# Kernel tuning notes

Measured on AMD Instinct MI355X. Metric: run time of the kernel, lower is better.

## Reference

```python
import jax, jax.numpy as jnp
import numpy as np

N = 100000      # nodes
E = 1600000     # edges (avg degree 16)
IN_DIM = 128
HID = 128
OUT = 10
EPS = 1e-5      # BatchNorm eps


def _lin(key, fan_in, fan_out):
    return jax.random.normal(key, (fan_in, fan_out), jnp.float32) * (1.0 / np.sqrt(fan_in))


def setup_inputs() -> dict:
    key = jax.random.key(0)
    ks = jax.random.split(key, 8)
    x = jax.random.normal(ks[0], (N, IN_DIM), jnp.float32)
    edge_index = jax.random.randint(ks[1], (2, E), 0, N, dtype=jnp.int64)
    return {
        "x": x,
        "edge_index": edge_index,
        "W0": _lin(ks[2], IN_DIM, HID), "b0": jnp.zeros((HID,), jnp.float32),
        "g0": jnp.ones((HID,), jnp.float32), "be0": jnp.zeros((HID,), jnp.float32),
        "W1": _lin(ks[3], HID, HID), "b1": jnp.zeros((HID,), jnp.float32),
        "g1": jnp.ones((HID,), jnp.float32), "be1": jnp.zeros((HID,), jnp.float32),
        "W2": _lin(ks[4], HID, OUT), "b2": jnp.zeros((OUT,), jnp.float32),
    }


def gcn_conv(x, W, b, src, dst, n):
    # PyG GCNConv: add self-loops, symmetric normalization D^-1/2 A D^-1/2.
    # deg includes the self-loop (+1).
    e = src.shape[0]
    deg = jax.ops.segment_sum(jnp.ones((e,), x.dtype), dst, num_segments=n) + 1.0
    dinv = jax.lax.rsqrt(deg)                     # deg >= 1 always
    norm = dinv[src] * dinv[dst]                  # [E]
    h = x @ W                                     # [N, out]
    msgs = h[src] * norm[:, None]                 # gather + scale, [E, out]
    agg = jax.ops.segment_sum(msgs, dst, num_segments=n)
    agg = agg + h * (dinv * dinv)[:, None]        # self-loop contribution
    return agg + b


def batch_norm(x, gamma, beta):
    mu = jnp.mean(x, axis=0)
    var = jnp.mean(jnp.square(x - mu), axis=0)    # biased var, as torch BN training
    return gamma * (x - mu) * jax.lax.rsqrt(var + EPS) + beta


def reference(x, edge_index, W0, b0, g0, be0, W1, b1, g1, be1, W2, b2):
    src, dst = edge_index[0], edge_index[1]
    h = jax.nn.relu(batch_norm(gcn_conv(x, W0, b0, src, dst, N), g0, be0))
    h = jax.nn.relu(batch_norm(gcn_conv(h, W1, b1, src, dst, N), g1, be1))
    return gcn_conv(h, W2, b2, src, dst, N)
```

## Files before the change

kernel.cpp:

```cpp
#include <hip/hip_runtime.h>
#include <hip/hip_bf16.h>

static constexpr int NN  = 100000;
static constexpr int NE  = 1600000;
static constexpr int DIM = 128;
static constexpr int OC  = 10;
static constexpr int BK  = 64;
static constexpr float BN_EPS = 1e-5f;
static constexpr float INVN   = 1.0f / (float)NN;

typedef unsigned short ushortT;
typedef unsigned int uintT;
typedef __attribute__((ext_vector_type(8))) short short8;
typedef __attribute__((ext_vector_type(4))) float floatx4;

__device__ __forceinline__ ushortT f2bf(float f) {
    union { float f; unsigned int i; } c;
    c.f = f;
    unsigned int r = c.i + 0x7FFFu + ((c.i >> 16) & 1u);
    return (ushortT)(r >> 16);
}

__device__ __forceinline__ uintT pack2(float lo, float hi) {
    return (uintT)f2bf(lo) | ((uintT)f2bf(hi) << 16);
}

__device__ __forceinline__ float4 f4fma(const float4 w, const float s, const float4 acc) {
    float4 r;
    r.x = fmaf(w.x, s, acc.x);
    r.y = fmaf(w.y, s, acc.y);
    r.z = fmaf(w.z, s, acc.z);
    r.w = fmaf(w.w, s, acc.w);
    return r;
}

__device__ __forceinline__ void acc8(const uint4 u, float* a) {
    a[0] += __uint_as_float(u.x << 16);
    a[1] += __uint_as_float(u.x & 0xFFFF0000u);
    a[2] += __uint_as_float(u.y << 16);
    a[3] += __uint_as_float(u.y & 0xFFFF0000u);
    a[4] += __uint_as_float(u.z << 16);
    a[5] += __uint_as_float(u.z & 0xFFFF0000u);
    a[6] += __uint_as_float(u.w << 16);
    a[7] += __uint_as_float(u.w & 0xFFFF0000u);
}

__device__ __forceinline__ void fma8(const uint4 u, float s, float* a) {
    a[0] = fmaf(__uint_as_float(u.x << 16),          s, a[0]);
    a[1] = fmaf(__uint_as_float(u.x & 0xFFFF0000u),  s, a[1]);
    a[2] = fmaf(__uint_as_float(u.y << 16),          s, a[2]);
    a[3] = fmaf(__uint_as_float(u.y & 0xFFFF0000u),  s, a[3]);
    a[4] = fmaf(__uint_as_float(u.z << 16),          s, a[4]);
    a[5] = fmaf(__uint_as_float(u.z & 0xFFFF0000u),  s, a[5]);
    a[6] = fmaf(__uint_as_float(u.w << 16),          s, a[6]);
    a[7] = fmaf(__uint_as_float(u.w & 0xFFFF0000u),  s, a[7]);
}

__device__ __forceinline__ void unp8(const uint4 u, float* a) {
    a[0] = __uint_as_float(u.x << 16);
    a[1] = __uint_as_float(u.x & 0xFFFF0000u);
    a[2] = __uint_as_float(u.y << 16);
    a[3] = __uint_as_float(u.y & 0xFFFF0000u);
    a[4] = __uint_as_float(u.z << 16);
    a[5] = __uint_as_float(u.z & 0xFFFF0000u);
    a[6] = __uint_as_float(u.w << 16);
    a[7] = __uint_as_float(u.w & 0xFFFF0000u);
}

__global__ void k_wt(const float* __restrict__ W0, const float* __restrict__ W1,
                     ushortT* __restrict__ WT0, ushortT* __restrict__ WT1,
                     float* __restrict__ stats) {
    int i = blockIdx.x * 256 + threadIdx.x;
    if (i < 512) stats[i] = 0.f;
    int half = i >> 14, r = i & 16383;
    int n = r >> 7, k = r & 127;
    if (half == 0) WT0[r] = f2bf(W0[k * 128 + n]);
    else           WT1[r] = f2bf(W1[k * 128 + n]);
}

__global__ __launch_bounds__(256, 8)
void k_fused(const int* __restrict__ src, const int* __restrict__ dst,
             int* __restrict__ cnt, int* __restrict__ bucket,
             const float* __restrict__ x, const ushortT* __restrict__ WT,
             ushortT* __restrict__ outb)
{
    const int idx = blockIdx.x;
    const int m = idx / 3, r3 = idx - 3 * m;
    if (r3 < 2) {
        int e = (2 * m + r3) * 256 + threadIdx.x;
        if (e < NE) {
            int t = dst[e];
            int slot = atomicAdd(&cnt[t], 1);
            if (slot < BK)
                __hip_atomic_store(&bucket[(size_t)t * BK + slot], src[e],
                                   __ATOMIC_RELAXED, __HIP_MEMORY_SCOPE_AGENT);
        }
        return;
    }
    __shared__ ushortT XS[32 * 136];
    const int tid  = threadIdx.x;
    const int row0 = m * 32;

    #pragma unroll
    for (int i = 0; i < 4; ++i) {
        int id2 = tid + 256 * i;
        int rr = id2 >> 5, c4 = id2 & 31;
        int grow = row0 + rr;
        float4 v = {0.f, 0.f, 0.f, 0.f};
        if (grow < NN) v = ((const float4*)(x + (size_t)grow * DIM))[c4];
        ushort4 o;
        o.x = f2bf(v.x); o.y = f2bf(v.y); o.z = f2bf(v.z); o.w = f2bf(v.w);
        *(ushort4*)(XS + rr * 136 + c4 * 4) = o;
    }
    __syncthreads();

    const int w    = tid >> 6;
    const int lane = tid & 63;
    const int q    = lane >> 4;
    const int mr   = lane & 15;
    const int rw   = (w >> 1) * 16;
    const int ch   = (w & 1) * 64;

    floatx4 acc[4];
    #pragma unroll
    for (int t = 0; t < 4; ++t) { acc[t][0] = 0.f; acc[t][1] = 0.f; acc[t][2] = 0.f; acc[t][3] = 0.f; }

    #pragma unroll
    for (int c = 0; c < 4; ++c) {
        short8 a = *(const short8*)(XS + (rw + mr) * 136 + c * 32 + q * 8);
        #pragma unroll
        for (int t = 0; t < 4; ++t) {
            short8 b = *(const short8*)(WT + (size_t)(ch + t * 16 + mr) * 128 + c * 32 + q * 8);
            acc[t] = __builtin_amdgcn_mfma_f32_16x16x32_bf16(a, b, acc[t], 0, 0, 0);
        }
    }

    #pragma unroll
    for (int rr = 0; rr < 4; ++rr) {
        int grow = row0 + rw + q * 4 + rr;
        if (grow < NN) {
            #pragma unroll
            for (int t = 0; t < 4; ++t)
                outb[(size_t)grow * DIM + ch + t * 16 + mr] = f2bf(acc[t][rr]);
        }
    }
}

__global__ void k_dinv(const int* __restrict__ cnt, float* __restrict__ dinv, int n) {
    int i = blockIdx.x * 256 + threadIdx.x;
    if (i < n) dinv[i] = rsqrtf((float)cnt[i] + 1.0f);
}

template <bool EDGE_SCALE>
__global__ __launch_bounds__(256)
void k_agg_wide(const ushortT* __restrict__ hb, const int* __restrict__ cnt,
                const int* __restrict__ bucket, const float* __restrict__ dinv,
                const float* __restrict__ bias, ushortT* __restrict__ outBb,
                float* __restrict__ stats)
{
    const int lane = threadIdx.x & 63;
    const int w    = threadIdx.x >> 6;
    const int sg   = lane >> 4;
    const int f    = lane & 15;
    const int wid  = blockIdx.x * 4 + w;
    const int nW   = gridDim.x * 4;
    const uint4* h4 = (const uint4*)hb;

    float bl[8];
    #pragma unroll
    for (int i = 0; i < 8; ++i) bl[i] = bias[f * 8 + i];

    float ssum[8], ssq[8];
    #pragma unroll
    for (int i = 0; i < 8; ++i) { ssum[i] = 0.f; ssq[i] = 0.f; }

    for (int n = wid; n < NN; n += nW) {
        int d = cnt[n];
        if (d > BK) d = BK;
        const int* bp = bucket + (size_t)n * BK;
        float a[8];
        #pragma unroll
        for (int i = 0; i < 8; ++i) a[i] = 0.f;

        int j = 0;
        for (; j + 8 <= d; j += 8) {
            int s0 = bp[j + sg];
            int s1 = bp[j + 4 + sg];
            uint4 u0 = h4[(size_t)s0 * 16 + f];
            uint4 u1 = h4[(size_t)s1 * 16 + f];
            if (EDGE_SCALE) {
                float d0 = dinv[s0], d1 = dinv[s1];
                fma8(u0, d0, a);
                fma8(u1, d1, a);
            } else {
                acc8(u0, a);
                acc8(u1, a);
            }
        }
        for (; j < d; j += 4) {
            int e = j + sg;
            if (e < d) {
                int s0 = bp[e];
                uint4 u = h4[(size_t)s0 * 16 + f];
                if (EDGE_SCALE) fma8(u, dinv[s0], a);
                else            acc8(u, a);
            }
        }
        #pragma unroll
        for (int i = 0; i < 8; ++i) {
            a[i] += __shfl_xor(a[i], 16);
            a[i] += __shfl_xor(a[i], 32);
        }
        if (lane < 16) {
            uint4 us = h4[(size_t)n * 16 + f];
            float di = dinv[n];
            if (EDGE_SCALE) fma8(us, di, a);
            else            acc8(us, a);
            float v[8];
            #pragma unroll
            for (int i = 0; i < 8; ++i) v[i] = fmaf(di, a[i], bl[i]);
            uint4 o;
            o.x = pack2(v[0], v[1]);
            o.y = pack2(v[2], v[3]);
            o.z = pack2(v[4], v[5]);
            o.w = pack2(v[6], v[7]);
            ((uint4*)(outBb + (size_t)n * DIM))[f] = o;
            #pragma unroll
            for (int i = 0; i < 8; ++i) {
                ssum[i] += v[i];
                ssq[i]  = fmaf(v[i], v[i], ssq[i]);
            }
        }
    }

    __shared__ float ls[4 * 128], lq[4 * 128];
    if (lane < 16) {
        #pragma unroll
        for (int i = 0; i < 8; ++i) {
            ls[w * 128 + f * 8 + i] = ssum[i];
            lq[w * 128 + f * 8 + i] = ssq[i];
        }
    }
    __syncthreads();
    int t = threadIdx.x;
    if (t < 128) {
        float a = ls[t] + ls[128 + t] + ls[256 + t] + ls[384 + t];
        float b = lq[t] + lq[128 + t] + lq[256 + t] + lq[384 + t];
        unsafeAtomicAdd(&stats[t], a);
        unsafeAtomicAdd(&stats[128 + t], b);
    }
}

__global__ __launch_bounds__(256)
void k_mm128_l1(const ushortT* __restrict__ inb, const ushortT* __restrict__ WT,
                const float* __restrict__ stats, const float* __restrict__ g,
                const float* __restrict__ be, const float* __restrict__ dinv,
                ushortT* __restrict__ outb)
{
    __shared__ ushortT XS[64 * 136];
    __shared__ float CA[128], CD[128];
    const int tid  = threadIdx.x;
    const int row0 = blockIdx.x * 64;

    if (tid < 128) {
        float mu  = stats[tid] * INVN;
        float var = stats[128 + tid] * INVN - mu * mu;
        float a = g[tid] * rsqrtf(var + BN_EPS);
        CA[tid] = a;
        CD[tid] = be[tid] - mu * a;
    }
    __syncthreads();

    #pragma unroll
    for (int i = 0; i < 4; ++i) {
        int idx = tid + 256 * i;
        int r = idx >> 4, c8 = idx & 15;
        int grow = row0 + r;
        uint4 u = {0, 0, 0, 0};
        if (grow < NN) u = ((const uint4*)(inb + (size_t)grow * DIM))[c8];
        float v[8];
        unp8(u, v);
        #pragma unroll
        for (int k = 0; k < 8; ++k)
            v[k] = fmaxf(0.f, fmaf(v[k], CA[c8 * 8 + k], CD[c8 * 8 + k]));
        uint4 o;
        o.x = pack2(v[0], v[1]);
        o.y = pack2(v[2], v[3]);
        o.z = pack2(v[4], v[5]);
        o.w = pack2(v[6], v[7]);
        *(uint4*)(XS + r * 136 + c8 * 8) = o;
    }
    __syncthreads();

    const int w    = tid >> 6;
    const int lane = tid & 63;
    const int q    = lane >> 4;
    const int mr   = lane & 15;
    const int rw   = w * 16;

    floatx4 acc[8];
    #pragma unroll
    for (int t = 0; t < 8; ++t) { acc[t][0] = 0.f; acc[t][1] = 0.f; acc[t][2] = 0.f; acc[t][3] = 0.f; }

    #pragma unroll
    for (int c = 0; c < 4; ++c) {
        short8 a = *(const short8*)(XS + (rw + mr) * 136 + c * 32 + q * 8);
        #pragma unroll
        for (int t = 0; t < 8; ++t) {
            short8 b = *(const short8*)(WT + (size_t)(t * 16 + mr) * 128 + c * 32 + q * 8);
            acc[t] = __builtin_amdgcn_mfma_f32_16x16x32_bf16(a, b, acc[t], 0, 0, 0);
        }
    }

    #pragma unroll
    for (int r = 0; r < 4; ++r) {
        int grow = row0 + rw + q * 4 + r;
        if (grow < NN) {
            float di = dinv[grow];
            #pragma unroll
            for (int t = 0; t < 8; ++t) {
                outb[(size_t)grow * DIM + t * 16 + mr] = f2bf(acc[t][r] * di);
            }
        }
    }
}

__global__ __launch_bounds__(128)
void k_mm_l2(const ushortT* __restrict__ inb, const float* __restrict__ W2,
             const float* __restrict__ stats, const float* __restrict__ g,
             const float* __restrict__ be, const float* __restrict__ dinv,
             ushortT* __restrict__ Cb)
{
    __shared__ float WL[128 * 16];
    __shared__ float XS[32 * 128];
    __shared__ float CA[128], CD[128];
    const int tid  = threadIdx.x;
    const int row0 = blockIdx.x * 32;

    {
        float mu  = stats[tid] * INVN;
        float var = stats[128 + tid] * INVN - mu * mu;
        float a = g[tid] * rsqrtf(var + BN_EPS);
        CA[tid] = a;
        CD[tid] = be[tid] - mu * a;
    }
    for (int idx = tid; idx < 128 * 16; idx += 128) {
        int k = idx >> 4, c = idx & 15;
        WL[idx] = (c < OC) ? W2[k * OC + c] : 0.0f;
    }
    __syncthreads();

    #pragma unroll
    for (int i = 0; i < 4; ++i) {
        int idx = tid + 128 * i;
        int r = idx >> 4, c8 = idx & 15;
        uint4 u = ((const uint4*)(inb + (size_t)(row0 + r) * DIM))[c8];
        float v[8];
        unp8(u, v);
        float* xp = XS + r * 128 + c8 * 8;
        #pragma unroll
        for (int k = 0; k < 8; ++k)
            xp[k] = fmaxf(0.f, fmaf(v[k], CA[c8 * 8 + k], CD[c8 * 8 + k]));
    }
    __syncthreads();

    const int cg = tid & 3;
    const int rg = tid >> 2;
    float4 acc = {0, 0, 0, 0};
    const float4* XS4 = (const float4*)XS;
    const float4* WL4 = (const float4*)WL;
    for (int k = 0; k < 128; k += 4) {
        float4 w0 = WL4[(k + 0) * 4 + cg];
        float4 w1 = WL4[(k + 1) * 4 + cg];
        float4 w2 = WL4[(k + 2) * 4 + cg];
        float4 w3 = WL4[(k + 3) * 4 + cg];
        float4 x = XS4[rg * 32 + (k >> 2)];
        acc = f4fma(w0, x.x, f4fma(w1, x.y, f4fma(w2, x.z, f4fma(w3, x.w, acc))));
    }
    float di = dinv[row0 + rg];
    uint2 o;
    o.x = pack2(acc.x * di, acc.y * di);
    o.y = pack2(acc.z * di, acc.w * di);
    ((uint2*)(Cb + ((size_t)row0 + rg) * 16))[cg] = o;
}

__global__ __launch_bounds__(256)
void k_agg10(const ushortT* __restrict__ Cb, const int* __restrict__ cnt,
             const int* __restrict__ bucket, const float* __restrict__ dinv,
             const float* __restrict__ b2, float* __restrict__ out)
{
    const int lane = threadIdx.x & 63;
    const int sg   = lane >> 3;
    const int f    = lane & 7;
    const int wid  = (blockIdx.x * 256 + threadIdx.x) >> 6;
    const int nW   = gridDim.x * 4;
    const uintT* Cu = (const uintT*)Cb;

    for (int n = wid; n < NN; n += nW) {
        int d = cnt[n];
        if (d > BK) d = BK;
        const int* bp = bucket + (size_t)n * BK;
        float a0 = 0.f, a1 = 0.f;
        for (int j = sg; j < d; j += 8) {
            uintT u = Cu[(size_t)bp[j] * 8 + f];
            a0 += __uint_as_float(u << 16);
            a1 += __uint_as_float(u & 0xFFFF0000u);
        }
        a0 += __shfl_xor(a0, 8);  a1 += __shfl_xor(a1, 8);
        a0 += __shfl_xor(a0, 16); a1 += __shfl_xor(a1, 16);
        a0 += __shfl_xor(a0, 32); a1 += __shfl_xor(a1, 32);
        if (lane < 8) {
            uintT us = Cu[(size_t)n * 8 + f];
            a0 += __uint_as_float(us << 16);
            a1 += __uint_as_float(us & 0xFFFF0000u);
            float di = dinv[n];
            if (2 * f < OC) {
                float2 o;
                o.x = fmaf(di, a0, b2[2 * f]);
                o.y = fmaf(di, a1, b2[2 * f + 1]);
                *(float2*)(out + (size_t)n * OC + 2 * f) = o;
            }
        }
    }
}

extern "C" void kernel_launch(void* const* d_in, const int* in_sizes, int n_in,
                              void* d_out, int out_size, void* d_ws, size_t ws_size,
                              hipStream_t stream) {
    const float* x    = (const float*)d_in[0];
    const int*   ei   = (const int*)d_in[1];
    const int*   srcv = ei;
    const int*   dstv = ei + NE;
    const float* W0  = (const float*)d_in[2];
    const float* b0  = (const float*)d_in[3];
    const float* g0  = (const float*)d_in[4];
    const float* be0 = (const float*)d_in[5];
    const float* W1  = (const float*)d_in[6];
    const float* b1  = (const float*)d_in[7];
    const float* g1  = (const float*)d_in[8];
    const float* be1 = (const float*)d_in[9];
    const float* W2  = (const float*)d_in[10];
    const float* b2  = (const float*)d_in[11];
    float* out = (float*)d_out;

    float* base   = (float*)d_ws;
    int*   cnt    = (int*)base;
    float* dinv   = base + NN;
    float* stats  = base + 2 * NN;
    ushortT* WT0  = (ushortT*)(base + 2 * NN + 512);
    ushortT* WT1  = (ushortT*)(base + 2 * NN + 8704);
    int*   bucket = (int*)(base + 2 * NN + 16896);
    ushortT* A_bf = (ushortT*)(base + 2 * NN + 16896 + (size_t)NN * BK);
    ushortT* B_bf = A_bf + (size_t)NN * DIM;
    ushortT* Cb   = A_bf;

    hipMemsetAsync(cnt, 0, NN * sizeof(int), stream);

    k_wt<<<128, 256, 0, stream>>>(W0, W1, WT0, WT1, stats);

    k_fused<<<9375, 256, 0, stream>>>(srcv, dstv, cnt, bucket, x, WT0, A_bf);
    k_dinv<<<(NN + 255) / 256, 256, 0, stream>>>(cnt, dinv, NN);

    k_agg_wide<true><<<2048, 256, 0, stream>>>(A_bf, cnt, bucket, dinv, b0, B_bf, stats);

    k_mm128_l1<<<(NN + 63) / 64, 256, 0, stream>>>(B_bf, WT1, stats, g0, be0, dinv, A_bf);
    k_agg_wide<false><<<2048, 256, 0, stream>>>(A_bf, cnt, bucket, dinv, b1, B_bf, stats + 256);

    k_mm_l2<<<NN / 32, 128, 0, stream>>>(B_bf, W2, stats + 256, g1, be1, dinv, Cb);
    k_agg10<<<1024, 256, 0, stream>>>(Cb, cnt, bucket, dinv, b2, out);
}
```

Measured before the change: 563.6 us.

## Split per-node edge counters into four sub-buckets to reduce atomic contention

```diff
diff --git a/kernel.cpp b/kernel.cpp
--- a/kernel.cpp
+++ b/kernel.cpp
@@ -5,7 +5,8 @@
 static constexpr int NE  = 1600000;
 static constexpr int DIM = 128;
 static constexpr int OC  = 10;
-static constexpr int BK  = 64;
+static constexpr int CAP   = 16;
+static constexpr int SLOTS = 80;
 static constexpr float BN_EPS = 1e-5f;
 static constexpr float INVN   = 1.0f / (float)NN;
 
@@ -67,20 +68,24 @@
     a[7] = __uint_as_float(u.w & 0xFFFF0000u);
 }
 
-__global__ void k_wt(const float* __restrict__ W0, const float* __restrict__ W1,
-                     ushortT* __restrict__ WT0, ushortT* __restrict__ WT1,
-                     float* __restrict__ stats) {
+__global__ void k_prep0(const float* __restrict__ W0, const float* __restrict__ W1,
+                        ushortT* __restrict__ WT0, ushortT* __restrict__ WT1,
+                        float* __restrict__ stats, int* __restrict__ cntAll) {
     int i = blockIdx.x * 256 + threadIdx.x;
+    for (int j = i; j < 5 * NN; j += 512 * 256) cntAll[j] = 0;
     if (i < 512) stats[i] = 0.f;
-    int half = i >> 14, r = i & 16383;
-    int n = r >> 7, k = r & 127;
-    if (half == 0) WT0[r] = f2bf(W0[k * 128 + n]);
-    else           WT1[r] = f2bf(W1[k * 128 + n]);
+    if (i < 32768) {
+        int half = i >> 14, r = i & 16383;
+        int n = r >> 7, k = r & 127;
+        if (half == 0) WT0[r] = f2bf(W0[k * 128 + n]);
+        else           WT1[r] = f2bf(W1[k * 128 + n]);
+    }
 }
 
 __global__ __launch_bounds__(256, 8)
 void k_fused(const int* __restrict__ src, const int* __restrict__ dst,
-             int* __restrict__ cnt, int* __restrict__ bucket,
+             int* __restrict__ cntR, int* __restrict__ cntOv,
+             int* __restrict__ bucket,
              const float* __restrict__ x, const ushortT* __restrict__ WT,
              ushortT* __restrict__ outb)
 {
@@ -90,9 +95,15 @@
         int e = (2 * m + r3) * 256 + threadIdx.x;
         if (e < NE) {
             int t = dst[e];
-            int slot = atomicAdd(&cnt[t], 1);
-            if (slot < BK)
-                __hip_atomic_store(&bucket[(size_t)t * BK + slot], src[e],
+            int r = e & 3;
+            int slot = atomicAdd(&cntR[(size_t)r * NN + t], 1);
+            int off = r * CAP + slot;
+            if (slot >= CAP) {
+                int s2 = atomicAdd(&cntOv[t], 1);
+                off = (s2 < CAP) ? (64 + s2) : -1;
+            }
+            if (off >= 0)
+                __hip_atomic_store(&bucket[(size_t)t * SLOTS + off], src[e],
                                    __ATOMIC_RELAXED, __HIP_MEMORY_SCOPE_AGENT);
         }
         return;
@@ -146,14 +157,23 @@
     }
 }
 
-__global__ void k_dinv(const int* __restrict__ cnt, float* __restrict__ dinv, int n) {
+__global__ void k_dinv(const int* __restrict__ cntR, const int* __restrict__ cntOv,
+                       float* __restrict__ dinv, uintT* __restrict__ pcnt) {
     int i = blockIdx.x * 256 + threadIdx.x;
-    if (i < n) dinv[i] = rsqrtf((float)cnt[i] + 1.0f);
+    if (i < NN) {
+        int c0 = cntR[i], c1 = cntR[NN + i], c2 = cntR[2 * NN + i], c3 = cntR[3 * NN + i];
+        int ov = cntOv[i];
+        dinv[i] = rsqrtf((float)(c0 + c1 + c2 + c3) + 1.0f);
+        c0 = min(c0, CAP); c1 = min(c1, CAP); c2 = min(c2, CAP); c3 = min(c3, CAP);
+        ov = min(ov, CAP);
+        pcnt[i] = (uintT)c0 | ((uintT)c1 << 5) | ((uintT)c2 << 10)
+                | ((uintT)c3 << 15) | ((uintT)ov << 20);
+    }
 }
 
 template <bool EDGE_SCALE>
 __global__ __launch_bounds__(256)
-void k_agg_wide(const ushortT* __restrict__ hb, const int* __restrict__ cnt,
+void k_agg_wide(const ushortT* __restrict__ hb, const uintT* __restrict__ pcnt,
                 const int* __restrict__ bucket, const float* __restrict__ dinv,
                 const float* __restrict__ bias, ushortT* __restrict__ outBb,
                 float* __restrict__ stats)
@@ -175,32 +195,18 @@
     for (int i = 0; i < 8; ++i) { ssum[i] = 0.f; ssq[i] = 0.f; }
 
     for (int n = wid; n < NN; n += nW) {
-        int d = cnt[n];
-        if (d > BK) d = BK;
-        const int* bp = bucket + (size_t)n * BK;
+        uintT pc = pcnt[n];
+        const int* bp = bucket + (size_t)n * SLOTS;
         float a[8];
         #pragma unroll
         for (int i = 0; i < 8; ++i) a[i] = 0.f;
 
-        int j = 0;
-        for (; j + 8 <= d; j += 8) {
-            int s0 = bp[j + sg];
-            int s1 = bp[j + 4 + sg];
-            uint4 u0 = h4[(size_t)s0 * 16 + f];
-            uint4 u1 = h4[(size_t)s1 * 16 + f];
-            if (EDGE_SCALE) {
-                float d0 = dinv[s0], d1 = dinv[s1];
-                fma8(u0, d0, a);
-                fma8(u1, d1, a);
-            } else {
-                acc8(u0, a);
-                acc8(u1, a);
-            }
-        }
-        for (; j < d; j += 4) {
-            int e = j + sg;
-            if (e < d) {
-                int s0 = bp[e];
+        #pragma unroll
+        for (int r = 0; r < 5; ++r) {
+            int d = (pc >> (5 * r)) & 31;
+            const int* sp = bp + r * CAP;
+            for (int j = sg; j < d; j += 4) {
+                int s0 = sp[j];
                 uint4 u = h4[(size_t)s0 * 16 + f];
                 if (EDGE_SCALE) fma8(u, dinv[s0], a);
                 else            acc8(u, a);
@@ -385,7 +391,7 @@
 }
 
 __global__ __launch_bounds__(256)
-void k_agg10(const ushortT* __restrict__ Cb, const int* __restrict__ cnt,
+void k_agg10(const ushortT* __restrict__ Cb, const uintT* __restrict__ pcnt,
              const int* __restrict__ bucket, const float* __restrict__ dinv,
              const float* __restrict__ b2, float* __restrict__ out)
 {
@@ -397,14 +403,18 @@
     const uintT* Cu = (const uintT*)Cb;
 
     for (int n = wid; n < NN; n += nW) {
-        int d = cnt[n];
-        if (d > BK) d = BK;
-        const int* bp = bucket + (size_t)n * BK;
+        uintT pc = pcnt[n];
+        const int* bp = bucket + (size_t)n * SLOTS;
         float a0 = 0.f, a1 = 0.f;
-        for (int j = sg; j < d; j += 8) {
-            uintT u = Cu[(size_t)bp[j] * 8 + f];
-            a0 += __uint_as_float(u << 16);
-            a1 += __uint_as_float(u & 0xFFFF0000u);
+        #pragma unroll
+        for (int r = 0; r < 5; ++r) {
+            int d = (pc >> (5 * r)) & 31;
+            const int* sp = bp + r * CAP;
+            for (int j = sg; j < d; j += 8) {
+                uintT u = Cu[(size_t)sp[j] * 8 + f];
+                a0 += __uint_as_float(u << 16);
+                a1 += __uint_as_float(u & 0xFFFF0000u);
+            }
         }
         a0 += __shfl_xor(a0, 8);  a1 += __shfl_xor(a1, 8);
         a0 += __shfl_xor(a0, 16); a1 += __shfl_xor(a1, 16);
@@ -444,28 +454,28 @@
     float* out = (float*)d_out;
 
     float* base   = (float*)d_ws;
-    int*   cnt    = (int*)base;
-    float* dinv   = base + NN;
-    float* stats  = base + 2 * NN;
-    ushortT* WT0  = (ushortT*)(base + 2 * NN + 512);
-    ushortT* WT1  = (ushortT*)(base + 2 * NN + 8704);
-    int*   bucket = (int*)(base + 2 * NN + 16896);
-    ushortT* A_bf = (ushortT*)(base + 2 * NN + 16896 + (size_t)NN * BK);
+    int*   cntR   = (int*)base;
+    int*   cntOv  = (int*)base + 4 * NN;
+    float* dinv   = base + 5 * NN;
+    uintT* pcnt   = (uintT*)(base + 6 * NN);
+    float* stats  = base + 7 * NN;
+    ushortT* WT0  = (ushortT*)(base + 7 * NN + 512);
+    ushortT* WT1  = (ushortT*)(base + 7 * NN + 8704);
+    int*   bucket = (int*)(base + 7 * NN + 16896);
+    ushortT* A_bf = (ushortT*)(base + 7 * NN + 16896 + (size_t)NN * SLOTS);
     ushortT* B_bf = A_bf + (size_t)NN * DIM;
     ushortT* Cb   = A_bf;
 
-    hipMemsetAsync(cnt, 0, NN * sizeof(int), stream);
-
-    k_wt<<<128, 256, 0, stream>>>(W0, W1, WT0, WT1, stats);
-
-    k_fused<<<9375, 256, 0, stream>>>(srcv, dstv, cnt, bucket, x, WT0, A_bf);
-    k_dinv<<<(NN + 255) / 256, 256, 0, stream>>>(cnt, dinv, NN);
-
-    k_agg_wide<true><<<2048, 256, 0, stream>>>(A_bf, cnt, bucket, dinv, b0, B_bf, stats);
+    k_prep0<<<512, 256, 0, stream>>>(W0, W1, WT0, WT1, stats, cntR);
+
+    k_fused<<<9375, 256, 0, stream>>>(srcv, dstv, cntR, cntOv, bucket, x, WT0, A_bf);
+    k_dinv<<<(NN + 255) / 256, 256, 0, stream>>>(cntR, cntOv, dinv, pcnt);
+
+    k_agg_wide<true><<<2048, 256, 0, stream>>>(A_bf, pcnt, bucket, dinv, b0, B_bf, stats);
 
     k_mm128_l1<<<(NN + 63) / 64, 256, 0, stream>>>(B_bf, WT1, stats, g0, be0, dinv, A_bf);
-    k_agg_wide<false><<<2048, 256, 0, stream>>>(A_bf, cnt, bucket, dinv, b1, B_bf, stats + 256);
+    k_agg_wide<false><<<2048, 256, 0, stream>>>(A_bf, pcnt, bucket, dinv, b1, B_bf, stats + 256);
 
     k_mm_l2<<<NN / 32, 128, 0, stream>>>(B_bf, W2, stats + 256, g1, be1, dinv, Cb);
-    k_agg10<<<1024, 256, 0, stream>>>(Cb, cnt, bucket, dinv, b2, out);
-}
+    k_agg10<<<1024, 256, 0, stream>>>(Cb, pcnt, bucket, dinv, b2, out);
+}
```

Result: slower. 642.9 us (+14.1%).
